# Kernel tuning notes

Hardware: AMD Instinct MI355X
Metric: run time of the kernel (lower is better)

## Reference

```python
import jax, jax.numpy as jnp
import numpy as np

D = 1024
H = 16
HD = D // H


def setup_inputs() -> dict:
    key = jax.random.key(0)
    ks = jax.random.split(key, 9)
    s = 1.0 / np.sqrt(D)
    x = jax.random.normal(ks[0], (2, 2048, D), dtype=jnp.float32)
    Wq = jax.random.uniform(ks[1], (D, D), jnp.float32, -s, s)
    bq = jax.random.uniform(ks[2], (D,), jnp.float32, -s, s)
    Wk = jax.random.uniform(ks[3], (D, D), jnp.float32, -s, s)
    bk = jax.random.uniform(ks[4], (D,), jnp.float32, -s, s)
    Wv = jax.random.uniform(ks[5], (D, D), jnp.float32, -s, s)
    bv = jax.random.uniform(ks[6], (D,), jnp.float32, -s, s)
    Wo = jax.random.uniform(ks[7], (D, D), jnp.float32, -s, s)
    bo = jax.random.uniform(ks[8], (D,), jnp.float32, -s, s)
    return {"x": x, "Wq": Wq, "bq": bq, "Wk": Wk, "bk": bk,
            "Wv": Wv, "bv": bv, "Wo": Wo, "bo": bo}


def reference(x, Wq, bq, Wk, bk, Wv, bv, Wo, bo):
    B, S, _ = x.shape
    # project and split heads -> [B, H, S, HD]
    def split(t):
        return t.reshape(B, S, H, HD).transpose(0, 2, 1, 3)
    q = split(x @ Wq + bq)
    k = split(x @ Wk + bk)
    v = split(x @ Wv + bv)
    scores = jnp.einsum('bhqd,bhkd->bhqk', q, k) / np.sqrt(HD).astype(np.float32)
    attn = jax.nn.softmax(scores, axis=-1)
    ctx = jnp.einsum('bhqk,bhkd->bhqd', attn, v)  # [B,H,S,HD]
    ctx = ctx.transpose(0, 2, 1, 3).reshape(B, S, D)
    return ctx @ Wo + bo
```

## Files before the change

kernel.cpp:

```cpp
#include <hip/hip_runtime.h>
#include <hip/hip_bf16.h>
#include <math.h>

#define BB 2
#define SS 2048
#define DD 1024
#define HH 16
#define HD 64
#define MM (BB * SS)

typedef __bf16 bf16;
typedef __attribute__((ext_vector_type(8))) __bf16 bf16x8;
typedef __attribute__((ext_vector_type(4))) __bf16 bf16x4;
typedef __attribute__((ext_vector_type(4))) float f32x4;
typedef __attribute__((ext_vector_type(4))) unsigned u32x4;

#define QSCL 0.18033688011112042f

__device__ __forceinline__ void glds16(const bf16* g, bf16* l) {
    __builtin_amdgcn_global_load_lds(
        (const __attribute__((address_space(1))) void*)g,
        (__attribute__((address_space(3))) void*)l, 16, 0, 0);
}

__device__ __forceinline__ unsigned cvtpk_bf16(float a, float b) {
    unsigned r;
    asm("v_cvt_pk_bf16_f32 %0, %1, %2" : "=v"(r) : "v"(a), "v"(b));
    return r;
}

__global__ __launch_bounds__(256) void cvt_x(const float* __restrict__ x,
                                             bf16* __restrict__ xb) {
    int i = (blockIdx.x * 256 + threadIdx.x) * 4;
    float4 v = *(const float4*)(x + i);
    bf16x4 o;
    o[0] = (bf16)v.x; o[1] = (bf16)v.y; o[2] = (bf16)v.z; o[3] = (bf16)v.w;
    *(bf16x4*)(xb + i) = o;
}

__global__ __launch_bounds__(256) void cvt_w(
    const float* __restrict__ W0, const float* __restrict__ W1,
    const float* __restrict__ W2, const float* __restrict__ W3,
    bf16* __restrict__ Wt) {
    const float* W = (blockIdx.z == 0) ? W0 : (blockIdx.z == 1) ? W1
                   : (blockIdx.z == 2) ? W2 : W3;
    bf16* dst = Wt + (size_t)blockIdx.z * DD * DD;

    __shared__ float T[64][65];
    int k0 = blockIdx.y * 64, n0 = blockIdx.x * 64;
    int tr = threadIdx.x >> 4, tc = (threadIdx.x & 15) * 4;
#pragma unroll
    for (int u = 0; u < 4; u++) {
        int r = tr + u * 16;
        float4 v = *(const float4*)&W[(size_t)(k0 + r) * DD + n0 + tc];
        T[tc + 0][r] = v.x; T[tc + 1][r] = v.y;
        T[tc + 2][r] = v.z; T[tc + 3][r] = v.w;
    }
    __syncthreads();
#pragma unroll
    for (int u = 0; u < 4; u++) {
        int r = tr + u * 16;
        bf16x4 o;
        o[0] = (bf16)T[r][tc + 0]; o[1] = (bf16)T[r][tc + 1];
        o[2] = (bf16)T[r][tc + 2]; o[3] = (bf16)T[r][tc + 3];
        *(bf16x4*)&dst[(size_t)(n0 + r) * DD + k0 + tc] = o;
    }
}

__global__ __launch_bounds__(256) void vt_kernel(const bf16* __restrict__ V,
                                                 bf16* __restrict__ Vt) {
    const int bh = blockIdx.y;
    const int b = bh >> 4, h = bh & 15;
    const int s0 = blockIdx.x * 64;

    __shared__ bf16 T[64][72];
    const int r = threadIdx.x >> 2;
    const int C = threadIdx.x & 3;
    const int c0 = C * 16;

    const bf16* src = V + ((size_t)(b * SS + s0 + r)) * DD + h * HD + c0;
    *(bf16x8*)&T[r][c0]     = *(const bf16x8*)(src);
    *(bf16x8*)&T[r][c0 + 8] = *(const bf16x8*)(src + 8);
    __syncthreads();

    const int M0 = (C >> 1) * 32 + (C & 1) * 8;
    bf16x8 o0, o1;
#pragma unroll
    for (int i = 0; i < 4; i++) o0[i]     = T[M0 + i][r];
#pragma unroll
    for (int i = 0; i < 4; i++) o0[4 + i] = T[M0 + 16 + i][r];
#pragma unroll
    for (int i = 0; i < 4; i++) o1[i]     = T[M0 + 4 + i][r];
#pragma unroll
    for (int i = 0; i < 4; i++) o1[4 + i] = T[M0 + 20 + i][r];
    bf16* dst = Vt + ((size_t)bh * HD + r) * SS + s0 + c0;
    *(bf16x8*)dst       = o0;
    *(bf16x8*)(dst + 8) = o1;
}

__global__ __launch_bounds__(256) void mfma_gemm(
    const bf16* __restrict__ A, const bf16* __restrict__ Wt0,
    const float* __restrict__ b0, const float* __restrict__ b1,
    const float* __restrict__ b2,
    bf16* __restrict__ o0, bf16* __restrict__ o1, bf16* __restrict__ o2) {
    const int z = blockIdx.z;
    const bf16* Wt = Wt0 + (size_t)z * DD * DD;
    const float* bias = (z == 0) ? b0 : (z == 1) ? b1 : b2;
    bf16* dstb = (z == 0) ? o0 : (z == 1) ? o1 : o2;
    const float scl = (z == 0) ? QSCL : 1.0f;

    __shared__ __align__(16) bf16 As[128 * 64];
    __shared__ __align__(16) bf16 Bs[128 * 64];

    const int tid = threadIdx.x;
    const int lane = tid & 63;
    const int w = tid >> 6;
    const int l15 = lane & 15, quad = lane >> 4;
    const int m0 = blockIdx.y * 128;
    const int n0 = blockIdx.x * 128;
    const int mw = (w & 1) * 64;
    const int nw = (w >> 1) * 64;

    f32x4 acc[4][4];
#pragma unroll
    for (int i = 0; i < 4; i++)
#pragma unroll
        for (int j = 0; j < 4; j++) acc[i][j] = (f32x4){0.f, 0.f, 0.f, 0.f};

    for (int kt = 0; kt < DD; kt += 64) {
        __syncthreads();
#pragma unroll
        for (int u = 0; u < 4; u++) {
            int j = tid + u * 256;
            int row = j >> 3, cp = j & 7;
            int c = cp ^ (row & 7);
            glds16(A  + (size_t)(m0 + row) * DD + kt + c * 8, &As[j * 8]);
            glds16(Wt + (size_t)(n0 + row) * DD + kt + c * 8, &Bs[j * 8]);
        }
        __syncthreads();

#pragma unroll
        for (int kh = 0; kh < 2; kh++) {
            bf16x8 af[4], bf[4];
#pragma unroll
            for (int i = 0; i < 4; i++) {
                int ra = mw + i * 16 + l15;
                int ja = ra * 8 + ((kh * 4 + quad) ^ (ra & 7));
                af[i] = *(const bf16x8*)&As[ja * 8];
                int rb = nw + i * 16 + l15;
                int jb = rb * 8 + ((kh * 4 + quad) ^ (rb & 7));
                bf[i] = *(const bf16x8*)&Bs[jb * 8];
            }
#pragma unroll
            for (int i = 0; i < 4; i++)
#pragma unroll
                for (int j = 0; j < 4; j++)
                    acc[i][j] = __builtin_amdgcn_mfma_f32_16x16x32_bf16(
                        af[i], bf[j], acc[i][j], 0, 0, 0);
        }
    }

    float bcol[4];
#pragma unroll
    for (int j = 0; j < 4; j++) bcol[j] = bias[n0 + nw + j * 16 + l15];

#pragma unroll
    for (int i = 0; i < 4; i++)
#pragma unroll
        for (int j = 0; j < 4; j++)
#pragma unroll
            for (int r = 0; r < 4; r++) {
                int row = m0 + mw + i * 16 + quad * 4 + r;
                int col = n0 + nw + j * 16 + l15;
                dstb[(size_t)row * DD + col] =
                    (bf16)((acc[i][j][r] + bcol[j]) * scl);
            }
}

__global__ __launch_bounds__(256) void mfma_gemm_out(
    const bf16* __restrict__ A, const bf16* __restrict__ Wt,
    const float* __restrict__ bias, float* __restrict__ out) {
    __shared__ __align__(16) bf16 As[64 * 64];
    __shared__ __align__(16) bf16 Bs[128 * 64];

    const int tid = threadIdx.x;
    const int lane = tid & 63;
    const int w = tid >> 6;
    const int l15 = lane & 15, quad = lane >> 4;
    const int m0 = blockIdx.y * 64;
    const int n0 = blockIdx.x * 128;
    const int mw = (w & 1) * 32;
    const int nw = (w >> 1) * 64;

    f32x4 acc[2][4];
#pragma unroll
    for (int i = 0; i < 2; i++)
#pragma unroll
        for (int j = 0; j < 4; j++) acc[i][j] = (f32x4){0.f, 0.f, 0.f, 0.f};

    for (int kt = 0; kt < DD; kt += 64) {
        __syncthreads();
#pragma unroll
        for (int u = 0; u < 2; u++) {
            int j = tid + u * 256;
            int row = j >> 3, c = (j & 7) ^ (row & 7);
            glds16(A + (size_t)(m0 + row) * DD + kt + c * 8, &As[j * 8]);
        }
#pragma unroll
        for (int u = 0; u < 4; u++) {
            int j = tid + u * 256;
            int row = j >> 3, c = (j & 7) ^ (row & 7);
            glds16(Wt + (size_t)(n0 + row) * DD + kt + c * 8, &Bs[j * 8]);
        }
        __syncthreads();

#pragma unroll
        for (int kh = 0; kh < 2; kh++) {
            bf16x8 af[2], bf[4];
#pragma unroll
            for (int i = 0; i < 2; i++) {
                int ra = mw + i * 16 + l15;
                int ja = ra * 8 + ((kh * 4 + quad) ^ (ra & 7));
                af[i] = *(const bf16x8*)&As[ja * 8];
            }
#pragma unroll
            for (int j = 0; j < 4; j++) {
                int rb = nw + j * 16 + l15;
                int jb = rb * 8 + ((kh * 4 + quad) ^ (rb & 7));
                bf[j] = *(const bf16x8*)&Bs[jb * 8];
            }
#pragma unroll
            for (int i = 0; i < 2; i++)
#pragma unroll
                for (int j = 0; j < 4; j++)
                    acc[i][j] = __builtin_amdgcn_mfma_f32_16x16x32_bf16(
                        af[i], bf[j], acc[i][j], 0, 0, 0);
        }
    }

    float bcol[4];
#pragma unroll
    for (int j = 0; j < 4; j++) bcol[j] = bias[n0 + nw + j * 16 + l15];

#pragma unroll
    for (int i = 0; i < 2; i++)
#pragma unroll
        for (int j = 0; j < 4; j++)
#pragma unroll
            for (int r = 0; r < 4; r++) {
                int row = m0 + mw + i * 16 + quad * 4 + r;
                int col = n0 + nw + j * 16 + l15;
                out[(size_t)row * DD + col] = acc[i][j][r] + bcol[j];
            }
}

__global__ __launch_bounds__(256) void mfma_attn(
    const bf16* __restrict__ Qb, const bf16* __restrict__ Kb,
    const bf16* __restrict__ Vtg, bf16* __restrict__ ctxb) {
    __shared__ __align__(16) bf16 Ks[2][64 * 64];
    __shared__ __align__(16) bf16 Vs[2][64 * 64];

    const int tid = threadIdx.x;
    const int lane = tid & 63;
    const int w = tid >> 6;
    const int l15 = lane & 15, quad = lane >> 4;
    const int bh = blockIdx.y;
    const int b = bh >> 4, h = bh & 15;
    const int q0 = blockIdx.x * 64;
    const size_t mb = (size_t)b * SS;
    const int hc = h * HD;
    const bf16* Vt_bh = Vtg + (size_t)bh * HD * SS;

    bf16x8 qf[2];
#pragma unroll
    for (int kh = 0; kh < 2; kh++)
        qf[kh] = *(const bf16x8*)&Qb[(mb + q0 + w * 16 + l15) * DD +
                                     hc + kh * 32 + quad * 8];

    bf16x8 onev;
#pragma unroll
    for (int i = 0; i < 8; i++) onev[i] = (bf16)1.0f;

    int koff[4][2], voff[4][2];
#pragma unroll
    for (int kb = 0; kb < 4; kb++) {
        int rk = kb * 16 + l15;
#pragma unroll
        for (int kh = 0; kh < 2; kh++)
            koff[kb][kh] = (rk * 8 + ((kh * 4 + quad) ^ (rk & 7))) * 8;
    }
#pragma unroll
    for (int nb = 0; nb < 4; nb++) {
        int rv = nb * 16 + l15;
#pragma unroll
        for (int kh = 0; kh < 2; kh++)
            voff[nb][kh] = (rv * 8 + ((kh * 4 + quad) ^ (rv & 7))) * 8;
    }

    const bf16* gK[2]; const bf16* gV[2]; int lo_[2];
#pragma unroll
    for (int u = 0; u < 2; u++) {
        int j = tid + u * 256;
        int row = j >> 3, cp = j & 7;
        int c = cp ^ (row & 7);
        gK[u] = Kb + (mb + row) * DD + hc + c * 8;
        gV[u] = Vt_bh + (size_t)row * SS + c * 8;
        lo_[u] = j * 8;
    }

    f32x4 o[4], lsum;
    lsum = (f32x4){0.f, 0.f, 0.f, 0.f};
#pragma unroll
    for (int nb = 0; nb < 4; nb++) o[nb] = (f32x4){0.f, 0.f, 0.f, 0.f};

#pragma unroll
    for (int u = 0; u < 2; u++) {
        glds16(gK[u], &Ks[0][lo_[u]]);  gK[u] += 64 * DD;
        glds16(gV[u], &Vs[0][lo_[u]]);  gV[u] += 64;
    }
    __syncthreads();

    for (int it = 0; it < SS / 64; ++it) {
        const int buf = it & 1;
        if (it + 1 < SS / 64) {
#pragma unroll
            for (int u = 0; u < 2; u++) {
                glds16(gK[u], &Ks[buf ^ 1][lo_[u]]);  gK[u] += 64 * DD;
                glds16(gV[u], &Vs[buf ^ 1][lo_[u]]);  gV[u] += 64;
            }
        }

        f32x4 sc[4];
#pragma unroll
        for (int kb = 0; kb < 4; kb++) sc[kb] = (f32x4){0.f, 0.f, 0.f, 0.f};
        __builtin_amdgcn_s_setprio(1);
#pragma unroll
        for (int kb = 0; kb < 4; kb++)
#pragma unroll
            for (int kh = 0; kh < 2; kh++) {
                bf16x8 kf = *(const bf16x8*)&Ks[buf][koff[kb][kh]];
                sc[kb] = __builtin_amdgcn_mfma_f32_16x16x32_bf16(
                    kf, qf[kh], sc[kb], 0, 0, 0);
            }
        __builtin_amdgcn_s_setprio(0);

        u32x4 pw[2];
#pragma unroll
        for (int kb = 0; kb < 4; kb++) {
            float p0 = exp2f(sc[kb][0]);
            float p1 = exp2f(sc[kb][1]);
            float p2 = exp2f(sc[kb][2]);
            float p3 = exp2f(sc[kb][3]);
            pw[kb >> 1][(kb & 1) * 2 + 0] = cvtpk_bf16(p0, p1);
            pw[kb >> 1][(kb & 1) * 2 + 1] = cvtpk_bf16(p2, p3);
        }
        bf16x8 pfr[2];
        pfr[0] = __builtin_bit_cast(bf16x8, pw[0]);
        pfr[1] = __builtin_bit_cast(bf16x8, pw[1]);

        __builtin_amdgcn_s_setprio(1);
#pragma unroll
        for (int kh = 0; kh < 2; kh++) {
            lsum = __builtin_amdgcn_mfma_f32_16x16x32_bf16(
                pfr[kh], onev, lsum, 0, 0, 0);
#pragma unroll
            for (int nb = 0; nb < 4; nb++) {
                bf16x8 vf = *(const bf16x8*)&Vs[buf][voff[nb][kh]];
                o[nb] = __builtin_amdgcn_mfma_f32_16x16x32_bf16(
                    pfr[kh], vf, o[nb], 0, 0, 0);
            }
        }
        __builtin_amdgcn_s_setprio(0);

        __syncthreads();
    }

    float li[4];
#pragma unroll
    for (int r = 0; r < 4; r++) li[r] = 1.0f / lsum[r];
#pragma unroll
    for (int nb = 0; nb < 4; nb++)
#pragma unroll
        for (int r = 0; r < 4; r++) {
            int qrow = q0 + w * 16 + quad * 4 + r;
            ctxb[(mb + qrow) * DD + hc + nb * 16 + l15] =
                (bf16)(o[nb][r] * li[r]);
        }
}

extern "C" void kernel_launch(void* const* d_in, const int* in_sizes, int n_in,
                              void* d_out, int out_size, void* d_ws, size_t ws_size,
                              hipStream_t stream) {
    const float* x  = (const float*)d_in[0];
    const float* Wq = (const float*)d_in[1];
    const float* bq = (const float*)d_in[2];
    const float* Wk = (const float*)d_in[3];
    const float* bk = (const float*)d_in[4];
    const float* Wv = (const float*)d_in[5];
    const float* bv = (const float*)d_in[6];
    const float* Wo = (const float*)d_in[7];
    const float* bo = (const float*)d_in[8];
    float* out = (float*)d_out;

    char* base = (char*)d_ws;
    bf16* xb   = (bf16*)(base);
    bf16* Wt   = (bf16*)(base + (8ull  << 20));
    bf16* Qb   = (bf16*)(base + (16ull << 20));
    bf16* Kb   = (bf16*)(base + (24ull << 20));
    bf16* Vb   = (bf16*)(base + (32ull << 20));
    bf16* ctxb = (bf16*)(base + (40ull << 20));
    bf16* Vtg  = xb;

    cvt_x<<<dim3((MM * DD) / (256 * 4)), dim3(256), 0, stream>>>(x, xb);
    cvt_w<<<dim3(16, 16, 4), dim3(256), 0, stream>>>(Wq, Wk, Wv, Wo, Wt);

    mfma_gemm<<<dim3(DD / 128, MM / 128, 3), dim3(256), 0, stream>>>(
        xb, Wt, bq, bk, bv, Qb, Kb, Vb);

    vt_kernel<<<dim3(SS / 64, BB * HH), dim3(256), 0, stream>>>(Vb, Vtg);

    mfma_attn<<<dim3(SS / 64, BB * HH), dim3(256), 0, stream>>>(Qb, Kb, Vtg, ctxb);

    mfma_gemm_out<<<dim3(DD / 128, MM / 64), dim3(256), 0, stream>>>(
        ctxb, Wt + 3ull * DD * DD, bo, out);
}
```

Baseline: 222.8 us.

## Software-pipeline QK^T of next tile with PV of current tile in attention loop

Restructures the attention inner loop so the scores for the next K tile are computed right after a barrier, in the same MFMA block as the PV product of the current tile, while exp2 of the current tile's scores runs earlier. The goal is to keep MFMA units busy and overlap the softmax VALU work with matrix ops, hiding latency between the two dependent GEMMs. It adds an extra __syncthreads per iteration and more live registers (two score sets), which could lower occupancy.

```diff
diff --git a/kernel.cpp b/kernel.cpp
--- a/kernel.cpp
+++ b/kernel.cpp
@@ -8,6 +8,7 @@
 #define HH 16
 #define HD 64
 #define MM (BB * SS)
+#define NT (SS / 64)
 
 typedef __bf16 bf16;
 typedef __attribute__((ext_vector_type(8))) __bf16 bf16x8;
@@ -320,9 +321,22 @@
     }
     __syncthreads();
 
-    for (int it = 0; it < SS / 64; ++it) {
-        const int buf = it & 1;
-        if (it + 1 < SS / 64) {
+    f32x4 scA[4];
+#pragma unroll
+    for (int kb = 0; kb < 4; kb++) scA[kb] = (f32x4){0.f, 0.f, 0.f, 0.f};
+#pragma unroll
+    for (int kb = 0; kb < 4; kb++)
+#pragma unroll
+        for (int kh = 0; kh < 2; kh++) {
+            bf16x8 kf = *(const bf16x8*)&Ks[0][koff[kb][kh]];
+            scA[kb] = __builtin_amdgcn_mfma_f32_16x16x32_bf16(
+                kf, qf[kh], scA[kb], 0, 0, 0);
+        }
+
+    int buf = 0;
+    for (int it = 0; it < NT; ++it) {
+        const bool more = (it + 1 < NT);
+        if (more) {
 #pragma unroll
             for (int u = 0; u < 2; u++) {
                 glds16(gK[u], &Ks[buf ^ 1][lo_[u]]);  gK[u] += 64 * DD;
@@ -330,27 +344,13 @@
             }
         }
 
-        f32x4 sc[4];
-#pragma unroll
-        for (int kb = 0; kb < 4; kb++) sc[kb] = (f32x4){0.f, 0.f, 0.f, 0.f};
-        __builtin_amdgcn_s_setprio(1);
-#pragma unroll
-        for (int kb = 0; kb < 4; kb++)
-#pragma unroll
-            for (int kh = 0; kh < 2; kh++) {
-                bf16x8 kf = *(const bf16x8*)&Ks[buf][koff[kb][kh]];
-                sc[kb] = __builtin_amdgcn_mfma_f32_16x16x32_bf16(
-                    kf, qf[kh], sc[kb], 0, 0, 0);
-            }
-        __builtin_amdgcn_s_setprio(0);
-
         u32x4 pw[2];
 #pragma unroll
         for (int kb = 0; kb < 4; kb++) {
-            float p0 = exp2f(sc[kb][0]);
-            float p1 = exp2f(sc[kb][1]);
-            float p2 = exp2f(sc[kb][2]);
-            float p3 = exp2f(sc[kb][3]);
+            float p0 = exp2f(scA[kb][0]);
+            float p1 = exp2f(scA[kb][1]);
+            float p2 = exp2f(scA[kb][2]);
+            float p3 = exp2f(scA[kb][3]);
             pw[kb >> 1][(kb & 1) * 2 + 0] = cvtpk_bf16(p0, p1);
             pw[kb >> 1][(kb & 1) * 2 + 1] = cvtpk_bf16(p2, p3);
         }
@@ -358,7 +358,22 @@
         pfr[0] = __builtin_bit_cast(bf16x8, pw[0]);
         pfr[1] = __builtin_bit_cast(bf16x8, pw[1]);
 
+        __syncthreads();
+
         __builtin_amdgcn_s_setprio(1);
+        f32x4 scB[4];
+#pragma unroll
+        for (int kb = 0; kb < 4; kb++) scB[kb] = (f32x4){0.f, 0.f, 0.f, 0.f};
+        if (more) {
+#pragma unroll
+            for (int kb = 0; kb < 4; kb++)
+#pragma unroll
+                for (int kh = 0; kh < 2; kh++) {
+                    bf16x8 kf = *(const bf16x8*)&Ks[buf ^ 1][koff[kb][kh]];
+                    scB[kb] = __builtin_amdgcn_mfma_f32_16x16x32_bf16(
+                        kf, qf[kh], scB[kb], 0, 0, 0);
+                }
+        }
 #pragma unroll
         for (int kh = 0; kh < 2; kh++) {
             lsum = __builtin_amdgcn_mfma_f32_16x16x32_bf16(
@@ -373,6 +388,10 @@
         __builtin_amdgcn_s_setprio(0);
 
         __syncthreads();
+
+#pragma unroll
+        for (int kb = 0; kb < 4; kb++) scA[kb] = scB[kb];
+        buf ^= 1;
     }
 
     float li[4];
```

Result: no change. 220.5 us (-1.0%).

## Software-pipeline attention QK/PV across tiles, polynomial exp2, merge conversion kernels

Applied to the files above, without the earlier changes.

Restructures the attention loop so the QK scores for the next K tile are computed while the PV product of the current tile is issued, using two score buffers and an unrolled-by-two loop. The aim is to overlap softmax ALU work with MFMA work and hide LDS latency. It also replaces exp2f with a degree-6 polynomial plus ldexp to avoid the transcendental unit. The x and weight bf16 conversion kernels are merged into one launch to remove a kernel launch. The extra barrier per half-iteration and higher register pressure could hurt occupancy.

```diff
diff --git a/kernel.cpp b/kernel.cpp
--- a/kernel.cpp
+++ b/kernel.cpp
@@ -8,6 +8,7 @@
 #define HH 16
 #define HD 64
 #define MM (BB * SS)
+#define NT (SS / 64)
 
 typedef __bf16 bf16;
 typedef __attribute__((ext_vector_type(8))) __bf16 bf16x8;
@@ -29,25 +30,39 @@
     return r;
 }
 
-__global__ __launch_bounds__(256) void cvt_x(const float* __restrict__ x,
-                                             bf16* __restrict__ xb) {
-    int i = (blockIdx.x * 256 + threadIdx.x) * 4;
-    float4 v = *(const float4*)(x + i);
-    bf16x4 o;
-    o[0] = (bf16)v.x; o[1] = (bf16)v.y; o[2] = (bf16)v.z; o[3] = (bf16)v.w;
-    *(bf16x4*)(xb + i) = o;
-}
-
-__global__ __launch_bounds__(256) void cvt_w(
+__device__ __forceinline__ float exp2p(float s) {
+    float n = rintf(s);
+    float f = s - n;
+    float p = 1.535336188319500e-4f;
+    p = fmaf(p, f, 1.339887440266574e-3f);
+    p = fmaf(p, f, 9.618437357674640e-3f);
+    p = fmaf(p, f, 5.550332471162809e-2f);
+    p = fmaf(p, f, 2.402264791363012e-1f);
+    p = fmaf(p, f, 6.931472028550421e-1f);
+    p = fmaf(p, f, 1.0f);
+    return ldexpf(p, (int)n);
+}
+
+__global__ __launch_bounds__(256) void cvt_prep(
+    const float* __restrict__ x, bf16* __restrict__ xb,
     const float* __restrict__ W0, const float* __restrict__ W1,
     const float* __restrict__ W2, const float* __restrict__ W3,
     bf16* __restrict__ Wt) {
-    const float* W = (blockIdx.z == 0) ? W0 : (blockIdx.z == 1) ? W1
-                   : (blockIdx.z == 2) ? W2 : W3;
-    bf16* dst = Wt + (size_t)blockIdx.z * DD * DD;
-
     __shared__ float T[64][65];
-    int k0 = blockIdx.y * 64, n0 = blockIdx.x * 64;
+    const int bid = blockIdx.x;
+    if (bid < 4096) {
+        int i = (bid * 256 + threadIdx.x) * 4;
+        float4 v = *(const float4*)(x + i);
+        bf16x4 o;
+        o[0] = (bf16)v.x; o[1] = (bf16)v.y; o[2] = (bf16)v.z; o[3] = (bf16)v.w;
+        *(bf16x4*)(xb + i) = o;
+        return;
+    }
+    const int b = bid - 4096;
+    const int z = b >> 8;
+    const float* W = (z == 0) ? W0 : (z == 1) ? W1 : (z == 2) ? W2 : W3;
+    bf16* dst = Wt + (size_t)z * DD * DD;
+    int k0 = ((b >> 4) & 15) * 64, n0 = (b & 15) * 64;
     int tr = threadIdx.x >> 4, tc = (threadIdx.x & 15) * 4;
 #pragma unroll
     for (int u = 0; u < 4; u++) {
@@ -280,6 +295,7 @@
     bf16x8 onev;
 #pragma unroll
     for (int i = 0; i < 8; i++) onev[i] = (bf16)1.0f;
+    const f32x4 zf = (f32x4){0.f, 0.f, 0.f, 0.f};
 
     int koff[4][2], voff[4][2];
 #pragma unroll
@@ -313,65 +329,77 @@
 #pragma unroll
     for (int nb = 0; nb < 4; nb++) o[nb] = (f32x4){0.f, 0.f, 0.f, 0.f};
 
-#pragma unroll
-    for (int u = 0; u < 2; u++) {
-        glds16(gK[u], &Ks[0][lo_[u]]);  gK[u] += 64 * DD;
-        glds16(gV[u], &Vs[0][lo_[u]]);  gV[u] += 64;
-    }
-    __syncthreads();
-
-    for (int it = 0; it < SS / 64; ++it) {
-        const int buf = it & 1;
-        if (it + 1 < SS / 64) {
-#pragma unroll
-            for (int u = 0; u < 2; u++) {
-                glds16(gK[u], &Ks[buf ^ 1][lo_[u]]);  gK[u] += 64 * DD;
-                glds16(gV[u], &Vs[buf ^ 1][lo_[u]]);  gV[u] += 64;
-            }
-        }
-
-        f32x4 sc[4];
-#pragma unroll
-        for (int kb = 0; kb < 4; kb++) sc[kb] = (f32x4){0.f, 0.f, 0.f, 0.f};
-        __builtin_amdgcn_s_setprio(1);
-#pragma unroll
-        for (int kb = 0; kb < 4; kb++)
-#pragma unroll
-            for (int kh = 0; kh < 2; kh++) {
-                bf16x8 kf = *(const bf16x8*)&Ks[buf][koff[kb][kh]];
-                sc[kb] = __builtin_amdgcn_mfma_f32_16x16x32_bf16(
-                    kf, qf[kh], sc[kb], 0, 0, 0);
-            }
-        __builtin_amdgcn_s_setprio(0);
-
+    auto STAGE = [&](int dbuf) {
+#pragma unroll
+        for (int u = 0; u < 2; u++) {
+            glds16(gK[u], &Ks[dbuf][lo_[u]]);  gK[u] += 64 * DD;
+            glds16(gV[u], &Vs[dbuf][lo_[u]]);  gV[u] += 64;
+        }
+    };
+    auto QK = [&](const bf16* Kbuf, f32x4 (&sc)[4]) {
+#pragma unroll
+        for (int kb = 0; kb < 4; kb++) {
+            bf16x8 kf0 = *(const bf16x8*)&Kbuf[koff[kb][0]];
+            bf16x8 kf1 = *(const bf16x8*)&Kbuf[koff[kb][1]];
+            sc[kb] = __builtin_amdgcn_mfma_f32_16x16x32_bf16(
+                kf0, qf[0], zf, 0, 0, 0);
+            sc[kb] = __builtin_amdgcn_mfma_f32_16x16x32_bf16(
+                kf1, qf[1], sc[kb], 0, 0, 0);
+        }
+    };
+    auto SM = [&](const f32x4 (&sc)[4], bf16x8 (&pfr)[2]) {
         u32x4 pw[2];
 #pragma unroll
         for (int kb = 0; kb < 4; kb++) {
-            float p0 = exp2f(sc[kb][0]);
-            float p1 = exp2f(sc[kb][1]);
-            float p2 = exp2f(sc[kb][2]);
-            float p3 = exp2f(sc[kb][3]);
+            float p0 = exp2p(sc[kb][0]);
+            float p1 = exp2p(sc[kb][1]);
+            float p2 = exp2p(sc[kb][2]);
+            float p3 = exp2p(sc[kb][3]);
             pw[kb >> 1][(kb & 1) * 2 + 0] = cvtpk_bf16(p0, p1);
             pw[kb >> 1][(kb & 1) * 2 + 1] = cvtpk_bf16(p2, p3);
         }
-        bf16x8 pfr[2];
         pfr[0] = __builtin_bit_cast(bf16x8, pw[0]);
         pfr[1] = __builtin_bit_cast(bf16x8, pw[1]);
-
-        __builtin_amdgcn_s_setprio(1);
+    };
+    auto PV = [&](const bf16x8 (&pfr)[2], const bf16* Vbuf) {
 #pragma unroll
         for (int kh = 0; kh < 2; kh++) {
             lsum = __builtin_amdgcn_mfma_f32_16x16x32_bf16(
                 pfr[kh], onev, lsum, 0, 0, 0);
 #pragma unroll
             for (int nb = 0; nb < 4; nb++) {
-                bf16x8 vf = *(const bf16x8*)&Vs[buf][voff[nb][kh]];
+                bf16x8 vf = *(const bf16x8*)&Vbuf[voff[nb][kh]];
                 o[nb] = __builtin_amdgcn_mfma_f32_16x16x32_bf16(
                     pfr[kh], vf, o[nb], 0, 0, 0);
             }
         }
+    };
+
+    STAGE(0);
+    __syncthreads();
+    f32x4 scA[4], scB[4];
+    QK(&Ks[0][0], scA);
+
+    for (int itp = 0; itp < NT / 2; ++itp) {
+        STAGE(1);
+        bf16x8 pfrA[2];
+        SM(scA, pfrA);
+        __syncthreads();
+        __builtin_amdgcn_s_setprio(1);
+        QK(&Ks[1][0], scB);
+        PV(pfrA, &Vs[0][0]);
         __builtin_amdgcn_s_setprio(0);
-
+        __syncthreads();
+
+        const bool moreB = (itp + 1 < NT / 2);
+        if (moreB) STAGE(0);
+        bf16x8 pfrB[2];
+        SM(scB, pfrB);
+        __syncthreads();
+        __builtin_amdgcn_s_setprio(1);
+        if (moreB) QK(&Ks[0][0], scA);
+        PV(pfrB, &Vs[1][0]);
+        __builtin_amdgcn_s_setprio(0);
         __syncthreads();
     }
 
@@ -411,8 +439,8 @@
     bf16* ctxb = (bf16*)(base + (40ull << 20));
     bf16* Vtg  = xb;
 
-    cvt_x<<<dim3((MM * DD) / (256 * 4)), dim3(256), 0, stream>>>(x, xb);
-    cvt_w<<<dim3(16, 16, 4), dim3(256), 0, stream>>>(Wq, Wk, Wv, Wo, Wt);
+    cvt_prep<<<dim3(4096 + 1024), dim3(256), 0, stream>>>(
+        x, xb, Wq, Wk, Wv, Wo, Wt);
 
     mfma_gemm<<<dim3(DD / 128, MM / 128, 3), dim3(256), 0, stream>>>(
         xb, Wt, bq, bk, bv, Qb, Kb, Vb);
```

Result: no change. 224.3 us (+0.7%).
